# Performance work log

Hardware: AMD Instinct MI355X
Metric: run time of the kernel (lower is better)

The kernel has to match this reference:

```python
import jax, jax.numpy as jnp
import numpy as np

N_EMBD = 2048
N_HEAD = 16
D_HEAD = N_EMBD // N_HEAD


def setup_inputs() -> dict:
    key = jax.random.key(0)
    k1, k2, k3 = jax.random.split(key, 3)
    x = jax.random.normal(k1, (2, 2048, N_EMBD), dtype=jnp.float32)
    # torch Linear stores weight as [out, in]; kept in that layout
    w_qkv = jax.random.normal(k2, (3 * N_EMBD, N_EMBD), dtype=jnp.float32) * (1.0 / np.sqrt(N_EMBD))
    w_out = jax.random.normal(k3, (N_EMBD, N_EMBD), dtype=jnp.float32) * (1.0 / np.sqrt(N_EMBD))
    return {"x": x, "w_qkv": w_qkv, "w_out": w_out}


def reference(x, w_qkv, w_out):
    B, T, C = x.shape
    H, D = N_HEAD, D_HEAD
    qkv = jnp.einsum('btc,oc->bto', x, w_qkv)            # [B,T,3C]
    qkv = qkv.reshape(B, T, 3, H, D)
    q = jnp.transpose(qkv[:, :, 0], (0, 2, 1, 3))        # [B,H,T,D]
    k = jnp.transpose(qkv[:, :, 1], (0, 2, 1, 3))
    v = jnp.transpose(qkv[:, :, 2], (0, 2, 1, 3))
    scale = 1.0 / np.sqrt(D).astype(np.float32)
    att = jnp.einsum('bhqd,bhkd->bhqk', q, k) * scale    # [B,H,T,T]
    causal = jnp.tril(jnp.ones((T, T), dtype=bool))
    att = jnp.where(causal[None, None], att, jnp.finfo(att.dtype).min)
    att = jax.nn.softmax(att, axis=-1)
    y = jnp.einsum('bhqk,bhkd->bhqd', att, v)            # [B,H,T,D]
    y = jnp.transpose(y, (0, 2, 1, 3)).reshape(B, T, C)
    return jnp.einsum('btc,oc->bto', y, w_out)
```

## Files before the change

### kernel.cpp

```cpp
#include <hip/hip_runtime.h>
#include <stdint.h>


typedef __attribute__((ext_vector_type(8))) short bf16x8;
typedef __attribute__((ext_vector_type(8))) unsigned short u16x8;
typedef __attribute__((ext_vector_type(4))) unsigned short u16x4;
typedef __attribute__((ext_vector_type(4))) float f32x4;

#define MFMA16(a, b, c) __builtin_amdgcn_mfma_f32_16x16x32_bf16((a), (b), (c), 0, 0, 0)

__device__ __forceinline__ unsigned short f2bf(float f) {
  union { float f; uint32_t u; } v; v.f = f;
  uint32_t r = v.u + 0x7FFFu + ((v.u >> 16) & 1u);
  return (unsigned short)(r >> 16);
}

__device__ __forceinline__ void gld_lds16(const unsigned short* g, unsigned short* lds) {
  __builtin_amdgcn_global_load_lds(
      (const __attribute__((address_space(1))) void*)g,
      (__attribute__((address_space(3))) void*)lds, 16, 0, 0);
}

__global__ __launch_bounds__(256) void cvt_bf16(const float* __restrict__ in,
                                                unsigned short* __restrict__ out, int n8) {
  int stride = gridDim.x * blockDim.x;
  for (int i = blockIdx.x * blockDim.x + threadIdx.x; i < n8; i += stride) {
    float4 a = reinterpret_cast<const float4*>(in)[i * 2];
    float4 b = reinterpret_cast<const float4*>(in)[i * 2 + 1];
    u16x8 o;
    o[0] = f2bf(a.x); o[1] = f2bf(a.y); o[2] = f2bf(a.z); o[3] = f2bf(a.w);
    o[4] = f2bf(b.x); o[5] = f2bf(b.y); o[6] = f2bf(b.z); o[7] = f2bf(b.w);
    reinterpret_cast<u16x8*>(out)[i] = o;
  }
}

#define STG128(BUFOFF, KOFF)                                                    \
  do {                                                                          \
    gld_lds16(gA0 + (KOFF), ldsA + (BUFOFF) + tid * 8);                         \
    gld_lds16(gA1 + (KOFF), ldsA + (BUFOFF) + 2048 + tid * 8);                  \
    gld_lds16(gB0 + (KOFF), ldsB + (BUFOFF) + tid * 8);                         \
    gld_lds16(gB1 + (KOFF), ldsB + (BUFOFF) + 2048 + tid * 8);                  \
  } while (0)

__device__ __forceinline__ void gemm128_step(const unsigned short* la,
                                             const unsigned short* lb,
                                             int wr, int wc, int fm, int fswz8,
                                             f32x4 acc[4][4]) {
  bf16x8 af[4], bfv[4];
#pragma unroll
  for (int i = 0; i < 4; i++)
    af[i] = *(const bf16x8*)&la[(wr + i * 16 + fm) * 32 + fswz8];
#pragma unroll
  for (int j = 0; j < 4; j++)
    bfv[j] = *(const bf16x8*)&lb[(wc + j * 16 + fm) * 32 + fswz8];
#pragma unroll
  for (int i = 0; i < 4; i++)
#pragma unroll
    for (int j = 0; j < 4; j++)
      acc[i][j] = MFMA16(af[i], bfv[j], acc[i][j]);
}

__device__ __forceinline__ void gemm128_dbuf(const unsigned short* __restrict__ A,
                                             const unsigned short* __restrict__ Bt,
                                             int K, int brow, int bcol,
                                             unsigned short* ldsA, unsigned short* ldsB,
                                             f32x4 acc[4][4]) {
  const int tid = threadIdx.x;
  const int l = tid & 63;
  const int w = tid >> 6;
  const int wr = (w >> 1) << 6;
  const int wc = (w & 1) << 6;

  const int srow = tid >> 2;
  const int sswz = (tid & 3) ^ ((srow >> 1) & 3);
  const unsigned short* gA0 = A + (size_t)(brow + srow) * K + 8 * sswz;
  const unsigned short* gA1 = gA0 + (size_t)64 * K;
  const unsigned short* gB0 = Bt + (size_t)(bcol + srow) * K + 8 * sswz;
  const unsigned short* gB1 = gB0 + (size_t)64 * K;

  const int fm = l & 15;
  const int fswz8 = 8 * ((l >> 4) ^ ((fm >> 1) & 3));

  STG128(0, 0);
  __syncthreads();

  for (int k0 = 0; k0 < K; k0 += 64) {
    STG128(4096, k0 + 32);
    gemm128_step(ldsA, ldsB, wr, wc, fm, fswz8, acc);
    __syncthreads();
    if (k0 + 64 < K) STG128(0, k0 + 64);
    gemm128_step(ldsA + 4096, ldsB + 4096, wr, wc, fm, fswz8, acc);
    __syncthreads();
  }
}

__global__ __launch_bounds__(256) void gemm_qkv(const unsigned short* __restrict__ xb,
                                                const unsigned short* __restrict__ wqb,
                                                unsigned short* __restrict__ Qb,
                                                unsigned short* __restrict__ Kb,
                                                unsigned short* __restrict__ Vtb) {
  __shared__ alignas(16) unsigned short ldsA[2 * 128 * 32];
  __shared__ alignas(16) unsigned short ldsB[2 * 128 * 32];
  f32x4 acc[4][4];
#pragma unroll
  for (int i = 0; i < 4; i++)
#pragma unroll
    for (int j = 0; j < 4; j++) acc[i][j] = (f32x4){0.f, 0.f, 0.f, 0.f};

  const int bid = blockIdx.x;
  const int xcd = bid & 7;
  const int loc = bid >> 3;
  const int bx = xcd * 6 + loc % 6;
  const int by = loc / 6;
  const int brow = by << 7;
  const int bcol = bx << 7;

  gemm128_dbuf(xb, wqb, 2048, brow, bcol, ldsA, ldsB, acc);

  const int l = threadIdx.x & 63;
  const int w = threadIdx.x >> 6;
  const int wr = (w >> 1) << 6, wc = (w & 1) << 6;
  const int which = bcol >> 11;
  const int bh = ((brow >> 11) << 4) | ((bcol >> 7) & 15);
  const int tbase = (brow & 2047) + wr + ((l >> 4) << 2);

#pragma unroll
  for (int i = 0; i < 4; i++) {
    const int t0 = tbase + i * 16;
#pragma unroll
    for (int j = 0; j < 4; j++) {
      const int d = wc + j * 16 + (l & 15);
      if (which == 2) {
        u16x4 pk;
#pragma unroll
        for (int r = 0; r < 4; r++) pk[r] = f2bf(acc[i][j][r]);
        *reinterpret_cast<u16x4*>(&Vtb[((size_t)bh * 128 + d) * 2048 + t0]) = pk;
      } else {
        unsigned short* dst = (which == 0 ? Qb : Kb) + ((size_t)bh * 2048 + t0) * 128 + d;
#pragma unroll
        for (int r = 0; r < 4; r++) dst[(size_t)r * 128] = f2bf(acc[i][j][r]);
      }
    }
  }
}

__global__ __launch_bounds__(256) void gemm_out(const unsigned short* __restrict__ yb,
                                                const unsigned short* __restrict__ wob,
                                                float* __restrict__ out) {
  __shared__ alignas(16) unsigned short ldsA[2 * 128 * 32];
  __shared__ alignas(16) unsigned short ldsB[2 * 128 * 32];
  f32x4 acc[4][4];
#pragma unroll
  for (int i = 0; i < 4; i++)
#pragma unroll
    for (int j = 0; j < 4; j++) acc[i][j] = (f32x4){0.f, 0.f, 0.f, 0.f};

  const int bid = blockIdx.x;
  const int xcd = bid & 7;
  const int loc = bid >> 3;
  const int bx = (xcd & 3) * 4 + (loc & 3);
  const int by = (xcd >> 2) * 16 + (loc >> 2);
  const int brow = by << 7;
  const int bcol = bx << 7;

  gemm128_dbuf(yb, wob, 2048, brow, bcol, ldsA, ldsB, acc);

  const int l = threadIdx.x & 63;
  const int w = threadIdx.x >> 6;
  const int wr = (w >> 1) << 6, wc = (w & 1) << 6;
#pragma unroll
  for (int i = 0; i < 4; i++) {
    const int m0 = brow + wr + i * 16 + ((l >> 4) << 2);
#pragma unroll
    for (int j = 0; j < 4; j++) {
      const int n = bcol + wc + j * 16 + (l & 15);
#pragma unroll
      for (int r = 0; r < 4; r++) out[(size_t)(m0 + r) * 2048 + n] = acc[i][j][r];
    }
  }
}

__global__ __launch_bounds__(256) void attn_kernel(const unsigned short* __restrict__ Qb,
                                                   const unsigned short* __restrict__ Kb,
                                                   const unsigned short* __restrict__ Vtb,
                                                   unsigned short* __restrict__ Yb) {
  __shared__ alignas(16) unsigned short lds_k[64 * 128];
  __shared__ alignas(16) unsigned short lds_v[128 * 64];
  __shared__ alignas(16) unsigned short p_lds[4][16 * 64];

  const int tid = threadIdx.x;
  const int l = tid & 63;
  const int w = tid >> 6;

  const int bid = blockIdx.x;
  const int xcd = bid & 7;
  const int loc = bid >> 3;
  const int bh = xcd * 4 + (loc >> 4);
  const int jidx = loc & 15;

  const int b = bh >> 4, h = bh & 15;
  const float SC = 0.12752585f;

  const unsigned short* Qg = Qb + (size_t)bh * 2048 * 128;
  const unsigned short* Kg = Kb + (size_t)bh * 2048 * 128;
  const unsigned short* Vg = Vtb + (size_t)bh * 128 * 2048;

  for (int ph = 0; ph < 2; ph++) {
    const int h64 = (ph == 0) ? jidx : (31 - jidx);
    const int q0 = h64 << 6;
    const int qw0 = q0 + (w << 4);

    bf16x8 qf[4];
#pragma unroll
    for (int ds = 0; ds < 4; ds++)
      qf[ds] = *(const bf16x8*)&Qg[(size_t)(qw0 + (l & 15)) * 128 + ds * 32 + 8 * (l >> 4)];

    f32x4 yacc[8];
#pragma unroll
    for (int dt = 0; dt < 8; dt++) yacc[dt] = (f32x4){0.f, 0.f, 0.f, 0.f};
    float mrow[4], lrow[4];
#pragma unroll
    for (int r = 0; r < 4; r++) { mrow[r] = -1e30f; lrow[r] = 0.f; }

    const int nkv = h64 + 1;
    for (int t = 0; t < nkv; t++) {
      const int kv0 = t << 6;
#pragma unroll
      for (int c = 0; c < 4; c++) {
        int s = c * 256 + tid;
        int row = s >> 4, g = s & 15;
        gld_lds16(&Kg[(size_t)(kv0 + row) * 128 + 8 * (g ^ (row & 7))], &lds_k[s * 8]);
      }
#pragma unroll
      for (int c = 0; c < 4; c++) {
        int s = c * 256 + tid;
        int row = s >> 3, g = s & 7;
        gld_lds16(&Vg[(size_t)row * 2048 + kv0 + 8 * (g ^ (row & 7))], &lds_v[s * 8]);
      }
      __syncthreads();

      if (kv0 <= qw0 + 15) {
        f32x4 sfr[4];
#pragma unroll
        for (int kt = 0; kt < 4; kt++) {
          const int kr = kt * 16 + (l & 15);
          f32x4 s4 = (f32x4){0.f, 0.f, 0.f, 0.f};
#pragma unroll
          for (int ds = 0; ds < 4; ds++) {
            bf16x8 kfr = *(const bf16x8*)&lds_k[kr * 128 + 8 * (((ds << 2) + (l >> 4)) ^ (kr & 7))];
            s4 = MFMA16(qf[ds], kfr, s4);
          }
          sfr[kt] = s4;
        }
        const bool need_mask = (kv0 + 63 > qw0);
#pragma unroll
        for (int kt = 0; kt < 4; kt++)
#pragma unroll
          for (int r = 0; r < 4; r++) {
            float sv = sfr[kt][r] * SC;
            if (need_mask) {
              int qa = qw0 + ((l >> 4) << 2) + r;
              int ka = kv0 + kt * 16 + (l & 15);
              sv = (ka > qa) ? -1e30f : sv;
            }
            sfr[kt][r] = sv;
          }
        float rmax, f[4], rsum[4];
#pragma unroll
        for (int r = 0; r < 4; r++) {
          rmax = fmaxf(fmaxf(sfr[0][r], sfr[1][r]), fmaxf(sfr[2][r], sfr[3][r]));
          rmax = fmaxf(rmax, __shfl_xor(rmax, 1));
          rmax = fmaxf(rmax, __shfl_xor(rmax, 2));
          rmax = fmaxf(rmax, __shfl_xor(rmax, 4));
          rmax = fmaxf(rmax, __shfl_xor(rmax, 8));
          float mn = fmaxf(mrow[r], rmax);
          f[r] = exp2f(mrow[r] - mn);
          mrow[r] = mn;
          rsum[r] = 0.f;
        }
#pragma unroll
        for (int kt = 0; kt < 4; kt++)
#pragma unroll
          for (int r = 0; r < 4; r++) {
            float p = exp2f(sfr[kt][r] - mrow[r]);
            rsum[r] += p;
            int row = ((l >> 4) << 2) + r;
            int k = kt * 16 + (l & 15);
            p_lds[w][row * 64 + (((k >> 3) ^ (row & 7)) << 3) + (k & 7)] = f2bf(p);
          }
#pragma unroll
        for (int r = 0; r < 4; r++) {
          float s = rsum[r];
          s += __shfl_xor(s, 1);
          s += __shfl_xor(s, 2);
          s += __shfl_xor(s, 4);
          s += __shfl_xor(s, 8);
          lrow[r] = lrow[r] * f[r] + s;
        }
#pragma unroll
        for (int dt = 0; dt < 8; dt++)
#pragma unroll
          for (int r = 0; r < 4; r++) yacc[dt][r] *= f[r];

        asm volatile("s_waitcnt lgkmcnt(0)" ::: "memory");
        __builtin_amdgcn_sched_barrier(0);

#pragma unroll
        for (int ks = 0; ks < 2; ks++) {
          const int prow = l & 15;
          bf16x8 pa = *(const bf16x8*)&p_lds[w][prow * 64 + ((((ks << 2) + (l >> 4)) ^ (prow & 7)) << 3)];
#pragma unroll
          for (int dt = 0; dt < 8; dt++) {
            const int d = dt * 16 + (l & 15);
            bf16x8 vb = *(const bf16x8*)&lds_v[d * 64 + ((((ks << 2) + (l >> 4)) ^ (d & 7)) << 3)];
            yacc[dt] = MFMA16(pa, vb, yacc[dt]);
          }
        }
      }
      __syncthreads();
    }
#pragma unroll
    for (int dt = 0; dt < 8; dt++)
#pragma unroll
      for (int r = 0; r < 4; r++) {
        int qa = qw0 + ((l >> 4) << 2) + r;
        Yb[((size_t)(b * 2048 + qa)) * 2048 + h * 128 + dt * 16 + (l & 15)] =
            f2bf(yacc[dt][r] / lrow[r]);
      }
  }
}

extern "C" void kernel_launch(void* const* d_in, const int* in_sizes, int n_in,
                              void* d_out, int out_size, void* d_ws, size_t ws_size,
                              hipStream_t stream) {
  const float* x    = (const float*)d_in[0];
  const float* wqkv = (const float*)d_in[1];
  const float* wout = (const float*)d_in[2];
  float* out = (float*)d_out;

  unsigned short* ws  = (unsigned short*)d_ws;
  unsigned short* xb  = ws;
  unsigned short* wqb = xb + (size_t)8388608;
  unsigned short* wob = wqb + (size_t)12582912;
  unsigned short* Qb  = wob + (size_t)4194304;
  unsigned short* Kb  = Qb + (size_t)8388608;
  unsigned short* Vtb = Kb + (size_t)8388608;
  unsigned short* Yb  = Vtb + (size_t)8388608;

  cvt_bf16<<<1024, 256, 0, stream>>>(x, xb, 8388608 / 8);
  cvt_bf16<<<1024, 256, 0, stream>>>(wqkv, wqb, 12582912 / 8);
  cvt_bf16<<<512, 256, 0, stream>>>(wout, wob, 4194304 / 8);
  gemm_qkv<<<1536, 256, 0, stream>>>(xb, wqb, Qb, Kb, Vtb);
  attn_kernel<<<512, 256, 0, stream>>>(Qb, Kb, Vtb, Yb);
  gemm_out<<<512, 256, 0, stream>>>(Yb, wob, out);
}
```

Before: 296.1 us.

## Double-buffer K tiles in attention and read V straight from global

The attention kernel now double-buffers K tiles in LDS, prefetching the next tile while the current one is computed. V is no longer staged through LDS; each wave loads its V fragments directly from global memory (through cache) right before the PV MFMAs. The GEMM main loop also peels its final iteration to drop a per-iteration branch. The aim is to hide K load latency and cut LDS traffic and footprint. The cost is that V is now read redundantly by all four waves with exposed global latency inside the inner loop.

```diff
diff --git a/kernel.cpp b/kernel.cpp
--- a/kernel.cpp
+++ b/kernel.cpp
@@ -84,14 +84,18 @@
   STG128(0, 0);
   __syncthreads();
 
-  for (int k0 = 0; k0 < K; k0 += 64) {
+  for (int k0 = 0; k0 < K - 64; k0 += 64) {
     STG128(4096, k0 + 32);
     gemm128_step(ldsA, ldsB, wr, wc, fm, fswz8, acc);
     __syncthreads();
-    if (k0 + 64 < K) STG128(0, k0 + 64);
+    STG128(0, k0 + 64);
     gemm128_step(ldsA + 4096, ldsB + 4096, wr, wc, fm, fswz8, acc);
     __syncthreads();
   }
+  STG128(4096, K - 32);
+  gemm128_step(ldsA, ldsB, wr, wc, fm, fswz8, acc);
+  __syncthreads();
+  gemm128_step(ldsA + 4096, ldsB + 4096, wr, wc, fm, fswz8, acc);
 }
 
 __global__ __launch_bounds__(256) void gemm_qkv(const unsigned short* __restrict__ xb,
@@ -180,12 +184,21 @@
   }
 }
 
+__device__ __forceinline__ void stage_k64(const unsigned short* __restrict__ Kg,
+                                          int kv0, unsigned short* dst, int tid) {
+#pragma unroll
+  for (int c = 0; c < 4; c++) {
+    int s = c * 256 + tid;
+    int row = s >> 4, g = s & 15;
+    gld_lds16(&Kg[(size_t)(kv0 + row) * 128 + 8 * (g ^ (row & 7))], &dst[s * 8]);
+  }
+}
+
 __global__ __launch_bounds__(256) void attn_kernel(const unsigned short* __restrict__ Qb,
                                                    const unsigned short* __restrict__ Kb,
                                                    const unsigned short* __restrict__ Vtb,
                                                    unsigned short* __restrict__ Yb) {
-  __shared__ alignas(16) unsigned short lds_k[64 * 128];
-  __shared__ alignas(16) unsigned short lds_v[128 * 64];
+  __shared__ alignas(16) unsigned short lds_k[2][64 * 128];
   __shared__ alignas(16) unsigned short p_lds[4][16 * 64];
 
   const int tid = threadIdx.x;
@@ -223,21 +236,15 @@
     for (int r = 0; r < 4; r++) { mrow[r] = -1e30f; lrow[r] = 0.f; }
 
     const int nkv = h64 + 1;
+
+    stage_k64(Kg, 0, lds_k[0], tid);
+    asm volatile("s_waitcnt vmcnt(0)" ::: "memory");
+    __syncthreads();
+
     for (int t = 0; t < nkv; t++) {
       const int kv0 = t << 6;
-#pragma unroll
-      for (int c = 0; c < 4; c++) {
-        int s = c * 256 + tid;
-        int row = s >> 4, g = s & 15;
-        gld_lds16(&Kg[(size_t)(kv0 + row) * 128 + 8 * (g ^ (row & 7))], &lds_k[s * 8]);
-      }
-#pragma unroll
-      for (int c = 0; c < 4; c++) {
-        int s = c * 256 + tid;
-        int row = s >> 3, g = s & 7;
-        gld_lds16(&Vg[(size_t)row * 2048 + kv0 + 8 * (g ^ (row & 7))], &lds_v[s * 8]);
-      }
-      __syncthreads();
+      const unsigned short* kb = lds_k[t & 1];
+      if (t + 1 < nkv) stage_k64(Kg, kv0 + 64, lds_k[(t & 1) ^ 1], tid);
 
       if (kv0 <= qw0 + 15) {
         f32x4 sfr[4];
@@ -247,7 +254,7 @@
           f32x4 s4 = (f32x4){0.f, 0.f, 0.f, 0.f};
 #pragma unroll
           for (int ds = 0; ds < 4; ds++) {
-            bf16x8 kfr = *(const bf16x8*)&lds_k[kr * 128 + 8 * (((ds << 2) + (l >> 4)) ^ (kr & 7))];
+            bf16x8 kfr = *(const bf16x8*)&kb[kr * 128 + 8 * (((ds << 2) + (l >> 4)) ^ (kr & 7))];
             s4 = MFMA16(qf[ds], kfr, s4);
           }
           sfr[kt] = s4;
@@ -307,16 +314,19 @@
 
 #pragma unroll
         for (int ks = 0; ks < 2; ks++) {
+          bf16x8 vbr[8];
+#pragma unroll
+          for (int dt = 0; dt < 8; dt++)
+            vbr[dt] = *(const bf16x8*)&Vg[(size_t)(dt * 16 + (l & 15)) * 2048 +
+                                          kv0 + ks * 32 + 8 * (l >> 4)];
           const int prow = l & 15;
           bf16x8 pa = *(const bf16x8*)&p_lds[w][prow * 64 + ((((ks << 2) + (l >> 4)) ^ (prow & 7)) << 3)];
 #pragma unroll
-          for (int dt = 0; dt < 8; dt++) {
-            const int d = dt * 16 + (l & 15);
-            bf16x8 vb = *(const bf16x8*)&lds_v[d * 64 + ((((ks << 2) + (l >> 4)) ^ (d & 7)) << 3)];
-            yacc[dt] = MFMA16(pa, vb, yacc[dt]);
-          }
+          for (int dt = 0; dt < 8; dt++)
+            yacc[dt] = MFMA16(pa, vbr[dt], yacc[dt]);
         }
       }
+      asm volatile("s_waitcnt vmcnt(0)" ::: "memory");
       __syncthreads();
     }
 #pragma unroll
```

Result: slower. 400.9 us (+35.4%).
